# Kernel tuning notes

Hardware: AMD Instinct MI355X
Metric: run time of the kernel (lower is better)

The kernel has to match this reference:

```python
import jax, jax.numpy as jnp
import numpy as np

B, S_ENC, S_DEC = 4, 2048, 1024
ENC_DIM, DEC_DIM, H = 1024, 1024, 16
CROSS_DIM = max(ENC_DIM, DEC_DIM)
HEAD_DIM_DEC = DEC_DIM // H
SCALE = HEAD_DIM_DEC ** 0.5  # module divides by dec_scaling only


def _linear_params(key, d_in, d_out):
    kw, kb = jax.random.split(key)
    bound = 1.0 / np.sqrt(d_in)
    W = jax.random.uniform(kw, (d_in, d_out), jnp.float32, -bound, bound)
    b = jax.random.uniform(kb, (d_out,), jnp.float32, -bound, bound)
    return W, b


def setup_inputs() -> dict:
    key = jax.random.key(0)
    ks = jax.random.split(key, 7)
    enc = jax.random.normal(ks[0], (B, S_ENC, ENC_DIM), jnp.float32)
    dec = jax.random.normal(ks[1], (B, S_DEC, DEC_DIM), jnp.float32)
    enc_mask = jax.random.uniform(ks[2], (B, 1, 1, S_ENC)) < 0.1
    q_w, q_b = _linear_params(ks[3], DEC_DIM, CROSS_DIM)
    k_w, k_b = _linear_params(ks[4], ENC_DIM, CROSS_DIM)
    v_w, v_b = _linear_params(ks[5], ENC_DIM, DEC_DIM)
    o_w, o_b = _linear_params(ks[6], DEC_DIM, DEC_DIM)
    return {"enc": enc, "enc_mask": enc_mask, "dec": dec,
            "q_w": q_w, "q_b": q_b, "k_w": k_w, "k_b": k_b,
            "v_w": v_w, "v_b": v_b, "o_w": o_w, "o_b": o_b}


def _split_heads(x):
    b, s, d = x.shape
    return x.reshape(b, s, H, d // H).transpose(0, 2, 1, 3)  # [b,h,s,hd]


def reference(enc, enc_mask, dec, q_w, q_b, k_w, k_b, v_w, v_b, o_w, o_b):
    q = _split_heads(dec @ q_w + q_b)   # [B,H,Sq,cross_hd]
    k = _split_heads(enc @ k_w + k_b)   # [B,H,Sk,cross_hd]
    v = _split_heads(enc @ v_w + v_b)   # [B,H,Sk,dec_hd]
    logits = jnp.einsum('bhqd,bhkd->bhqk', q, k) / SCALE
    logits = jnp.where(enc_mask, -jnp.inf, logits)
    a = jax.nn.softmax(logits, axis=-1)
    x = jnp.einsum('bhqk,bhkd->bhqd', a, v)          # [B,H,Sq,dec_hd]
    x = x.transpose(0, 2, 1, 3).reshape(x.shape[0], x.shape[2], -1)  # [B,Sq,DEC_DIM]
    return x @ o_w + o_b
```

## Files before the change

### kernel.cpp

```cpp
#include <hip/hip_runtime.h>
#include <hip/hip_bf16.h>
#include <cstdint>

#define BB   4
#define SENC 2048
#define SDEC 1024
#define DM   1024
#define NH   16
#define HD   64

using short8 = __attribute__((ext_vector_type(8))) short;
using f32x4  = __attribute__((ext_vector_type(4))) float;

__device__ inline unsigned short f2bf(float f) {
    return (unsigned short)((__builtin_bit_cast(unsigned int, f) + 0x8000u) >> 16);
}

__device__ inline float fexp2(float x) {
#if __has_builtin(__builtin_amdgcn_exp2f)
    return __builtin_amdgcn_exp2f(x);
#else
    return exp2f(x);
#endif
}

#if __has_builtin(__builtin_amdgcn_global_load_lds)
#define HAS_GLL 1
#endif

__device__ inline void stage16(const void* g, void* l) {
#ifdef HAS_GLL
    typedef __attribute__((address_space(1))) const unsigned int guint;
    typedef __attribute__((address_space(3))) unsigned int luint;
    __builtin_amdgcn_global_load_lds((guint*)g, (luint*)l, 16, 0, 0);
#else
    *(short8*)l = *(const short8*)g;
#endif
}

__global__ __launch_bounds__(256) void cvt_kernel(const float* __restrict__ in,
                                                  unsigned short* __restrict__ out, int n) {
    int i = (blockIdx.x * 256 + threadIdx.x) * 4;
    if (i >= n) return;
    float4 v = *(const float4*)(in + i);
    ushort4 o;
    o.x = f2bf(v.x); o.y = f2bf(v.y); o.z = f2bf(v.z); o.w = f2bf(v.w);
    *(ushort4*)(out + i) = o;
}

__global__ __launch_bounds__(256) void mask_cvt_kernel(const int* __restrict__ m,
                                                       float* __restrict__ mf, int n) {
    int i = blockIdx.x * 256 + threadIdx.x;
    if (i < n) mf[i] = m[i] ? -1e30f : 0.0f;
}

__global__ __launch_bounds__(256) void wtrans_kernel(
    const float* __restrict__ qw, const float* __restrict__ kw,
    const float* __restrict__ vw, const float* __restrict__ ow,
    unsigned short* __restrict__ qwt, unsigned short* __restrict__ kwt,
    unsigned short* __restrict__ vwt, unsigned short* __restrict__ owt) {
    const float* src; unsigned short* dst;
    switch (blockIdx.z) {
        case 0:  src = qw; dst = qwt; break;
        case 1:  src = kw; dst = kwt; break;
        case 2:  src = vw; dst = vwt; break;
        default: src = ow; dst = owt; break;
    }
    __shared__ float t[64][65];
    const int k0 = blockIdx.y * 64, n0 = blockIdx.x * 64;
    const int tid = threadIdx.x;
    #pragma unroll
    for (int it = 0; it < 16; ++it) {
        int e = it * 256 + tid, r = e >> 6, c = e & 63;
        t[r][c] = src[(size_t)(k0 + r) * DM + n0 + c];
    }
    __syncthreads();
    #pragma unroll
    for (int it = 0; it < 16; ++it) {
        int e = it * 256 + tid, r = e >> 6, c = e & 63;
        dst[(size_t)(n0 + r) * DM + k0 + c] = f2bf(t[c][r]);
    }
}

template <int MODE>
__global__ __launch_bounds__(256) void gemm_bt(const unsigned short* __restrict__ A,
                                               const unsigned short* __restrict__ Bt,
                                               const float* __restrict__ bias,
                                               void* __restrict__ Cout) {
    __shared__ unsigned short As[128 * 32];
    __shared__ unsigned short Bs[128 * 32];
    const int tid = threadIdx.x;
    const int wave = tid >> 6, lane = tid & 63, quad = lane >> 4, l16 = lane & 15;
    const int wr = wave >> 1, wc = wave & 1;
    const int m0 = blockIdx.y * 128, n0 = blockIdx.x * 128;
    const int r16 = lane >> 2, c8 = (lane & 3) * 8;
    f32x4 acc[4][4] = {};
    for (int kb = 0; kb < DM; kb += 32) {
        #pragma unroll
        for (int i = 0; i < 2; ++i) {
            const int row = wave * 32 + i * 16 + r16;
            stage16(&A[(size_t)(m0 + row) * DM + kb + c8], &As[row * 32 + c8]);
            stage16(&Bt[(size_t)(n0 + row) * DM + kb + c8], &Bs[row * 32 + c8]);
        }
        __syncthreads();
        short8 af[4], bfr[4];
        #pragma unroll
        for (int i = 0; i < 4; ++i) af[i] = *(const short8*)&As[(wr * 64 + i * 16 + l16) * 32 + quad * 8];
        #pragma unroll
        for (int j = 0; j < 4; ++j) bfr[j] = *(const short8*)&Bs[(wc * 64 + j * 16 + l16) * 32 + quad * 8];
        #pragma unroll
        for (int i = 0; i < 4; ++i)
            #pragma unroll
            for (int j = 0; j < 4; ++j)
                acc[i][j] = __builtin_amdgcn_mfma_f32_16x16x32_bf16(af[i], bfr[j], acc[i][j], 0, 0, 0);
        __syncthreads();
    }
    #pragma unroll
    for (int i = 0; i < 4; ++i) {
        #pragma unroll
        for (int j = 0; j < 4; ++j) {
            const int gc = n0 + wc * 64 + j * 16 + l16;
            const float bv = bias[gc];
            #pragma unroll
            for (int rr = 0; rr < 4; ++rr) {
                const int gr = m0 + wr * 64 + i * 16 + quad * 4 + rr;
                float v = acc[i][j][rr] + bv;
                if (MODE == 0) {
                    int b = gr >> 10, sq = gr & 1023, h = gc >> 6, d = gc & 63;
                    ((unsigned short*)Cout)[(((size_t)(b * NH + h) * SDEC + sq) << 6) + d] = f2bf(v * 0.18033688011112042f);
                } else if (MODE == 1) {
                    int b = gr >> 11, sk = gr & 2047, h = gc >> 6, d = gc & 63;
                    ((unsigned short*)Cout)[(((size_t)(b * NH + h) * SENC + sk) << 6) + d] = f2bf(v);
                } else if (MODE == 2) {
                    int b = gr >> 11, sk = gr & 2047, h = gc >> 6, d = gc & 63;
                    ((unsigned short*)Cout)[((size_t)(b * NH + h) * HD + d) * SENC + sk] = f2bf(v);
                } else {
                    ((float*)Cout)[(size_t)gr * DM + gc] = v;
                }
            }
        }
    }
}

__global__ __launch_bounds__(512) void attn_kernel(const unsigned short* __restrict__ Qb,
                                                   const unsigned short* __restrict__ Kb,
                                                   const unsigned short* __restrict__ Vtb,
                                                   const float* __restrict__ maskf,
                                                   unsigned short* __restrict__ Xb) {
    __shared__ unsigned short Ks[64 * 72];
    __shared__ unsigned short Vs[64 * 72];
    __shared__ unsigned short Ps[8][16 * 72];
    const int bh = blockIdx.y, b = bh >> 4, h = bh & 15;
    const int q0 = blockIdx.x * 128;
    const int tid = threadIdx.x, wave = tid >> 6, lane = tid & 63, quad = lane >> 4, l16 = lane & 15;

    const unsigned short* Qp = Qb + ((size_t)bh * SDEC + q0 + wave * 16) * HD;
    short8 qf0 = *(const short8*)&Qp[l16 * HD + quad * 8];
    short8 qf1 = *(const short8*)&Qp[l16 * HD + 32 + quad * 8];

    const unsigned short* Kp = Kb + (size_t)bh * SENC * HD;
    const unsigned short* Vp = Vtb + (size_t)bh * HD * SENC;
    const float* mp = maskf + (size_t)b * SENC;

    float lsum[4] = {0.f, 0.f, 0.f, 0.f};
    f32x4 o[4] = {};
    const int srow = tid >> 3, scol = (tid & 7) * 8;

    for (int kb = 0; kb < SENC; kb += 64) {
        *(short8*)&Ks[srow * 72 + scol] = *(const short8*)&Kp[(size_t)(kb + srow) * HD + scol];
        *(short8*)&Vs[srow * 72 + scol] = *(const short8*)&Vp[(size_t)srow * SENC + kb + scol];
        __syncthreads();
        f32x4 s[4];
        #pragma unroll
        for (int j = 0; j < 4; ++j) {
            short8 b0 = *(const short8*)&Ks[(j * 16 + l16) * 72 + quad * 8];
            short8 b1 = *(const short8*)&Ks[(j * 16 + l16) * 72 + 32 + quad * 8];
            f32x4 c = {};
            c = __builtin_amdgcn_mfma_f32_16x16x32_bf16(qf0, b0, c, 0, 0, 0);
            c = __builtin_amdgcn_mfma_f32_16x16x32_bf16(qf1, b1, c, 0, 0, 0);
            s[j] = c;
        }
        float mk[4];
        #pragma unroll
        for (int j = 0; j < 4; ++j) mk[j] = mp[kb + j * 16 + l16];
        #pragma unroll
        for (int rr = 0; rr < 4; ++rr) {
            #pragma unroll
            for (int j = 0; j < 4; ++j) {
                float p = fexp2(s[j][rr] + mk[j]);
                lsum[rr] += p;
                Ps[wave][(quad * 4 + rr) * 72 + j * 16 + l16] = f2bf(p);
            }
        }
        asm volatile("s_waitcnt lgkmcnt(0)" ::: "memory");
        short8 pf0 = *(const short8*)&Ps[wave][l16 * 72 + quad * 8];
        short8 pf1 = *(const short8*)&Ps[wave][l16 * 72 + 32 + quad * 8];
        #pragma unroll
        for (int j = 0; j < 4; ++j) {
            short8 v0 = *(const short8*)&Vs[(j * 16 + l16) * 72 + quad * 8];
            short8 v1 = *(const short8*)&Vs[(j * 16 + l16) * 72 + 32 + quad * 8];
            o[j] = __builtin_amdgcn_mfma_f32_16x16x32_bf16(pf0, v0, o[j], 0, 0, 0);
            o[j] = __builtin_amdgcn_mfma_f32_16x16x32_bf16(pf1, v1, o[j], 0, 0, 0);
        }
        __syncthreads();
    }
    float inv[4];
    #pragma unroll
    for (int rr = 0; rr < 4; ++rr) {
        float l = lsum[rr];
        #pragma unroll
        for (int d = 1; d < 16; d <<= 1) l += __shfl_xor(l, d);
        inv[rr] = 1.0f / l;
    }
    #pragma unroll
    for (int j = 0; j < 4; ++j)
        #pragma unroll
        for (int rr = 0; rr < 4; ++rr) {
            int sq = q0 + wave * 16 + quad * 4 + rr;
            Xb[((size_t)(b * SDEC) + sq) * DM + h * HD + j * 16 + l16] = f2bf(o[j][rr] * inv[rr]);
        }
}

extern "C" void kernel_launch(void* const* d_in, const int* in_sizes, int n_in,
                              void* d_out, int out_size, void* d_ws, size_t ws_size,
                              hipStream_t stream) {
    const float* enc   = (const float*)d_in[0];
    const int*   emask = (const int*)d_in[1];
    const float* dec   = (const float*)d_in[2];
    const float* q_w   = (const float*)d_in[3];
    const float* q_b   = (const float*)d_in[4];
    const float* k_w   = (const float*)d_in[5];
    const float* k_b   = (const float*)d_in[6];
    const float* v_w   = (const float*)d_in[7];
    const float* v_b   = (const float*)d_in[8];
    const float* o_w   = (const float*)d_in[9];
    const float* o_b   = (const float*)d_in[10];
    float* out = (float*)d_out;

    char* ws = (char*)d_ws;
    unsigned short* decb = (unsigned short*)ws; ws += (size_t)4096 * 1024 * 2;
    unsigned short* encb = (unsigned short*)ws; ws += (size_t)8192 * 1024 * 2;
    unsigned short* qwt  = (unsigned short*)ws; ws += (size_t)1024 * 1024 * 2;
    unsigned short* kwt  = (unsigned short*)ws; ws += (size_t)1024 * 1024 * 2;
    unsigned short* vwt  = (unsigned short*)ws; ws += (size_t)1024 * 1024 * 2;
    unsigned short* owt  = (unsigned short*)ws; ws += (size_t)1024 * 1024 * 2;
    unsigned short* Qb   = (unsigned short*)ws; ws += (size_t)BB * NH * SDEC * HD * 2;
    unsigned short* Kb   = (unsigned short*)ws; ws += (size_t)BB * NH * SENC * HD * 2;
    unsigned short* Vtb  = (unsigned short*)ws; ws += (size_t)BB * NH * HD * SENC * 2;
    unsigned short* Xb   = (unsigned short*)ws; ws += (size_t)4096 * 1024 * 2;
    float*          mkf  = (float*)ws;          ws += (size_t)BB * SENC * 4;

    cvt_kernel<<<4096, 256, 0, stream>>>(dec, decb, 4096 * 1024);
    cvt_kernel<<<8192, 256, 0, stream>>>(enc, encb, 8192 * 1024);
    mask_cvt_kernel<<<32, 256, 0, stream>>>(emask, mkf, BB * SENC);
    wtrans_kernel<<<dim3(16, 16, 4), 256, 0, stream>>>(q_w, k_w, v_w, o_w, qwt, kwt, vwt, owt);
    gemm_bt<0><<<dim3(8, 32), 256, 0, stream>>>(decb, qwt, q_b, (void*)Qb);
    gemm_bt<1><<<dim3(8, 64), 256, 0, stream>>>(encb, kwt, k_b, (void*)Kb);
    gemm_bt<2><<<dim3(8, 64), 256, 0, stream>>>(encb, vwt, v_b, (void*)Vtb);
    attn_kernel<<<dim3(8, 64), 512, 0, stream>>>(Qb, Kb, Vtb, mkf, Xb);
    gemm_bt<3><<<dim3(8, 32), 256, 0, stream>>>(Xb, owt, o_b, (void*)out);
}
```

Before: 300.2 us.

## Merge QKV GEMMs and conversions, double-buffer attention with two query groups per wave

Merges the dec and enc conversions into one launch and folds the mask conversion into the attention kernel, which now reads the int mask directly. The Q, K and V projections become a single launch of 1280 blocks over a concatenated K/V weight. Attention now runs 256 threads, each wave handling 32 query rows against K/V tiles that are double-buffered in LDS via global_load_lds. P is written with packed bf16 stores, and softmax row sums are reduced with fewer shuffles. The aim is to cut launch count and per-tile load latency, at the cost of more registers per wave and a different LDS layout that may conflict.

Result: no change. 299.8 us (-0.1%).

```diff
diff --git a/kernel.cpp b/kernel.cpp
--- a/kernel.cpp
+++ b/kernel.cpp
@@ -14,6 +14,10 @@
 
 __device__ inline unsigned short f2bf(float f) {
     return (unsigned short)((__builtin_bit_cast(unsigned int, f) + 0x8000u) >> 16);
+}
+__device__ inline unsigned int pk2bf(float a, float b) {
+    return ((__builtin_bit_cast(unsigned int, a) + 0x8000u) >> 16) |
+           ((__builtin_bit_cast(unsigned int, b) + 0x8000u) & 0xffff0000u);
 }
 
 __device__ inline float fexp2(float x) {
@@ -38,32 +42,28 @@
 #endif
 }
 
-__global__ __launch_bounds__(256) void cvt_kernel(const float* __restrict__ in,
-                                                  unsigned short* __restrict__ out, int n) {
+__global__ __launch_bounds__(256) void cvt2_kernel(const float* __restrict__ dec,
+                                                   const float* __restrict__ enc,
+                                                   unsigned short* __restrict__ out) {
+    const int nd = BB * SDEC * DM;
     int i = (blockIdx.x * 256 + threadIdx.x) * 4;
-    if (i >= n) return;
-    float4 v = *(const float4*)(in + i);
+    const float* src = (i < nd) ? (dec + i) : (enc + (i - nd));
+    float4 v = *(const float4*)src;
     ushort4 o;
     o.x = f2bf(v.x); o.y = f2bf(v.y); o.z = f2bf(v.z); o.w = f2bf(v.w);
     *(ushort4*)(out + i) = o;
 }
 
-__global__ __launch_bounds__(256) void mask_cvt_kernel(const int* __restrict__ m,
-                                                       float* __restrict__ mf, int n) {
-    int i = blockIdx.x * 256 + threadIdx.x;
-    if (i < n) mf[i] = m[i] ? -1e30f : 0.0f;
-}
-
 __global__ __launch_bounds__(256) void wtrans_kernel(
     const float* __restrict__ qw, const float* __restrict__ kw,
     const float* __restrict__ vw, const float* __restrict__ ow,
-    unsigned short* __restrict__ qwt, unsigned short* __restrict__ kwt,
-    unsigned short* __restrict__ vwt, unsigned short* __restrict__ owt) {
+    unsigned short* __restrict__ qwt, unsigned short* __restrict__ kvwt,
+    unsigned short* __restrict__ owt) {
     const float* src; unsigned short* dst;
     switch (blockIdx.z) {
         case 0:  src = qw; dst = qwt; break;
-        case 1:  src = kw; dst = kwt; break;
-        case 2:  src = vw; dst = vwt; break;
+        case 1:  src = kw; dst = kvwt; break;
+        case 2:  src = vw; dst = kvwt + (size_t)1024 * DM; break;
         default: src = ow; dst = owt; break;
     }
     __shared__ float t[64][65];
@@ -82,13 +82,76 @@
     }
 }
 
-template <int MODE>
-__global__ __launch_bounds__(256) void gemm_bt(const unsigned short* __restrict__ A,
-                                               const unsigned short* __restrict__ Bt,
-                                               const float* __restrict__ bias,
-                                               void* __restrict__ Cout) {
-    __shared__ unsigned short As[128 * 32];
-    __shared__ unsigned short Bs[128 * 32];
+__global__ __launch_bounds__(256) void gemm_qkv_kernel(
+    const unsigned short* __restrict__ encb, const unsigned short* __restrict__ decb,
+    const unsigned short* __restrict__ kvwt, const unsigned short* __restrict__ qwt,
+    const float* __restrict__ q_b, const float* __restrict__ k_b, const float* __restrict__ v_b,
+    unsigned short* __restrict__ Qb, unsigned short* __restrict__ Kb,
+    unsigned short* __restrict__ Vtb) {
+    __shared__ __align__(16) unsigned short As[128 * 32];
+    __shared__ __align__(16) unsigned short Bs[128 * 32];
+    const int id = blockIdx.x;
+    const bool isKV = id < 1024;
+    const unsigned short *A, *Bt;
+    int m0, n0;
+    if (isKV) { A = encb; Bt = kvwt; m0 = (id >> 4) * 128; n0 = (id & 15) * 128; }
+    else      { int i2 = id - 1024; A = decb; Bt = qwt; m0 = (i2 >> 3) * 128; n0 = (i2 & 7) * 128; }
+    const int tid = threadIdx.x;
+    const int wave = tid >> 6, lane = tid & 63, quad = lane >> 4, l16 = lane & 15;
+    const int wr = wave >> 1, wc = wave & 1;
+    const int r16 = lane >> 2, c8 = (lane & 3) * 8;
+    f32x4 acc[4][4] = {};
+    for (int kb = 0; kb < DM; kb += 32) {
+        #pragma unroll
+        for (int i = 0; i < 2; ++i) {
+            const int row = wave * 32 + i * 16 + r16;
+            stage16(&A[(size_t)(m0 + row) * DM + kb + c8], &As[row * 32 + c8]);
+            stage16(&Bt[(size_t)(n0 + row) * DM + kb + c8], &Bs[row * 32 + c8]);
+        }
+        __syncthreads();
+        short8 af[4], bfr[4];
+        #pragma unroll
+        for (int i = 0; i < 4; ++i) af[i] = *(const short8*)&As[(wr * 64 + i * 16 + l16) * 32 + quad * 8];
+        #pragma unroll
+        for (int j = 0; j < 4; ++j) bfr[j] = *(const short8*)&Bs[(wc * 64 + j * 16 + l16) * 32 + quad * 8];
+        #pragma unroll
+        for (int i = 0; i < 4; ++i)
+            #pragma unroll
+            for (int j = 0; j < 4; ++j)
+                acc[i][j] = __builtin_amdgcn_mfma_f32_16x16x32_bf16(af[i], bfr[j], acc[i][j], 0, 0, 0);
+        __syncthreads();
+    }
+    #pragma unroll
+    for (int i = 0; i < 4; ++i) {
+        #pragma unroll
+        for (int j = 0; j < 4; ++j) {
+            const int gc = n0 + wc * 64 + j * 16 + l16;
+            #pragma unroll
+            for (int rr = 0; rr < 4; ++rr) {
+                const int gr = m0 + wr * 64 + i * 16 + quad * 4 + rr;
+                if (!isKV) {
+                    int b = gr >> 10, sq = gr & 1023, h = gc >> 6, d = gc & 63;
+                    float v = (acc[i][j][rr] + q_b[gc]) * 0.18033688011112042f;
+                    Qb[(((size_t)(b * NH + h) * SDEC + sq) << 6) + d] = f2bf(v);
+                } else if (gc < 1024) {
+                    int b = gr >> 11, sk = gr & 2047, h = gc >> 6, d = gc & 63;
+                    Kb[(((size_t)(b * NH + h) * SENC + sk) << 6) + d] = f2bf(acc[i][j][rr] + k_b[gc]);
+                } else {
+                    int gc2 = gc & 1023;
+                    int b = gr >> 11, sk = gr & 2047, h = gc2 >> 6, d = gc2 & 63;
+                    Vtb[((size_t)(b * NH + h) * HD + d) * SENC + sk] = f2bf(acc[i][j][rr] + v_b[gc2]);
+                }
+            }
+        }
+    }
+}
+
+__global__ __launch_bounds__(256) void gemm_o_kernel(const unsigned short* __restrict__ A,
+                                                     const unsigned short* __restrict__ Bt,
+                                                     const float* __restrict__ bias,
+                                                     float* __restrict__ Cout) {
+    __shared__ __align__(16) unsigned short As[128 * 32];
+    __shared__ __align__(16) unsigned short Bs[128 * 32];
     const int tid = threadIdx.x;
     const int wave = tid >> 6, lane = tid & 63, quad = lane >> 4, l16 = lane & 15;
     const int wr = wave >> 1, wc = wave & 1;
@@ -116,7 +179,7 @@
         __syncthreads();
     }
     #pragma unroll
-    for (int i = 0; i < 4; ++i) {
+    for (int i = 0; i < 4; ++i)
         #pragma unroll
         for (int j = 0; j < 4; ++j) {
             const int gc = n0 + wc * 64 + j * 16 + l16;
@@ -124,101 +187,120 @@
             #pragma unroll
             for (int rr = 0; rr < 4; ++rr) {
                 const int gr = m0 + wr * 64 + i * 16 + quad * 4 + rr;
-                float v = acc[i][j][rr] + bv;
-                if (MODE == 0) {
-                    int b = gr >> 10, sq = gr & 1023, h = gc >> 6, d = gc & 63;
-                    ((unsigned short*)Cout)[(((size_t)(b * NH + h) * SDEC + sq) << 6) + d] = f2bf(v * 0.18033688011112042f);
-                } else if (MODE == 1) {
-                    int b = gr >> 11, sk = gr & 2047, h = gc >> 6, d = gc & 63;
-                    ((unsigned short*)Cout)[(((size_t)(b * NH + h) * SENC + sk) << 6) + d] = f2bf(v);
-                } else if (MODE == 2) {
-                    int b = gr >> 11, sk = gr & 2047, h = gc >> 6, d = gc & 63;
-                    ((unsigned short*)Cout)[((size_t)(b * NH + h) * HD + d) * SENC + sk] = f2bf(v);
-                } else {
-                    ((float*)Cout)[(size_t)gr * DM + gc] = v;
-                }
-            }
-        }
-    }
-}
-
-__global__ __launch_bounds__(512) void attn_kernel(const unsigned short* __restrict__ Qb,
-                                                   const unsigned short* __restrict__ Kb,
-                                                   const unsigned short* __restrict__ Vtb,
-                                                   const float* __restrict__ maskf,
-                                                   unsigned short* __restrict__ Xb) {
-    __shared__ unsigned short Ks[64 * 72];
-    __shared__ unsigned short Vs[64 * 72];
-    __shared__ unsigned short Ps[8][16 * 72];
+                Cout[(size_t)gr * DM + gc] = acc[i][j][rr] + bv;
+            }
+        }
+}
+
+__global__ __launch_bounds__(256, 2) void attn_kernel(const unsigned short* __restrict__ Qb,
+                                                      const unsigned short* __restrict__ Kb,
+                                                      const unsigned short* __restrict__ Vtb,
+                                                      const int* __restrict__ mask,
+                                                      unsigned short* __restrict__ Xb) {
+    __shared__ __align__(16) unsigned short Ks[2][2][64 * 32];
+    __shared__ __align__(16) unsigned short Vs[2][2][64 * 32];
+    __shared__ __align__(16) unsigned short Ps[4][16 * 72];
     const int bh = blockIdx.y, b = bh >> 4, h = bh & 15;
     const int q0 = blockIdx.x * 128;
-    const int tid = threadIdx.x, wave = tid >> 6, lane = tid & 63, quad = lane >> 4, l16 = lane & 15;
-
-    const unsigned short* Qp = Qb + ((size_t)bh * SDEC + q0 + wave * 16) * HD;
-    short8 qf0 = *(const short8*)&Qp[l16 * HD + quad * 8];
-    short8 qf1 = *(const short8*)&Qp[l16 * HD + 32 + quad * 8];
+    const int tid = threadIdx.x, wave = tid >> 6, lane = tid & 63;
+    const int quad = lane >> 4, l16 = lane & 15;
+    const int sr = lane >> 2, sc = (lane & 3) * 8;
 
     const unsigned short* Kp = Kb + (size_t)bh * SENC * HD;
     const unsigned short* Vp = Vtb + (size_t)bh * HD * SENC;
-    const float* mp = maskf + (size_t)b * SENC;
-
-    float lsum[4] = {0.f, 0.f, 0.f, 0.f};
-    f32x4 o[4] = {};
-    const int srow = tid >> 3, scol = (tid & 7) * 8;
-
-    for (int kb = 0; kb < SENC; kb += 64) {
-        *(short8*)&Ks[srow * 72 + scol] = *(const short8*)&Kp[(size_t)(kb + srow) * HD + scol];
-        *(short8*)&Vs[srow * 72 + scol] = *(const short8*)&Vp[(size_t)srow * SENC + kb + scol];
-        __syncthreads();
-        f32x4 s[4];
+    const int* mp = mask + (size_t)b * SENC;
+
+    short8 qf[2][2];
+    {
+        const unsigned short* Qp = Qb + ((size_t)bh * SDEC + q0 + wave * 32) * HD;
+        #pragma unroll
+        for (int g = 0; g < 2; ++g) {
+            qf[g][0] = *(const short8*)&Qp[(g * 16 + l16) * HD + quad * 8];
+            qf[g][1] = *(const short8*)&Qp[(g * 16 + l16) * HD + 32 + quad * 8];
+        }
+    }
+
+    float lsum[2] = {0.f, 0.f};
+    f32x4 o[2][4] = {};
+
+    {
+        const unsigned short* kg = Kp + (size_t)(wave * 16 + sr) * HD;
+        stage16(kg + sc,      &Ks[0][0][(wave * 16 + sr) * 32 + sc]);
+        stage16(kg + 32 + sc, &Ks[0][1][(wave * 16 + sr) * 32 + sc]);
+        const unsigned short* vg = Vp + (size_t)(wave * 16 + sr) * SENC;
+        stage16(vg + sc,      &Vs[0][0][(wave * 16 + sr) * 32 + sc]);
+        stage16(vg + 32 + sc, &Vs[0][1][(wave * 16 + sr) * 32 + sc]);
+    }
+
+    for (int it = 0; it < SENC / 64; ++it) {
+        const int bf = it & 1;
+        __syncthreads();
+        if (it + 1 < SENC / 64) {
+            const int nb = bf ^ 1, kb2 = (it + 1) * 64;
+            const unsigned short* kg = Kp + (size_t)(kb2 + wave * 16 + sr) * HD;
+            stage16(kg + sc,      &Ks[nb][0][(wave * 16 + sr) * 32 + sc]);
+            stage16(kg + 32 + sc, &Ks[nb][1][(wave * 16 + sr) * 32 + sc]);
+            const unsigned short* vg = Vp + (size_t)(wave * 16 + sr) * SENC + kb2;
+            stage16(vg + sc,      &Vs[nb][0][(wave * 16 + sr) * 32 + sc]);
+            stage16(vg + 32 + sc, &Vs[nb][1][(wave * 16 + sr) * 32 + sc]);
+        }
+        const int kb = it * 64;
+        short8 kA0[4], kA1[4], vB0[4], vB1[4];
         #pragma unroll
         for (int j = 0; j < 4; ++j) {
-            short8 b0 = *(const short8*)&Ks[(j * 16 + l16) * 72 + quad * 8];
-            short8 b1 = *(const short8*)&Ks[(j * 16 + l16) * 72 + 32 + quad * 8];
-            f32x4 c = {};
-            c = __builtin_amdgcn_mfma_f32_16x16x32_bf16(qf0, b0, c, 0, 0, 0);
-            c = __builtin_amdgcn_mfma_f32_16x16x32_bf16(qf1, b1, c, 0, 0, 0);
-            s[j] = c;
-        }
-        float mk[4];
-        #pragma unroll
-        for (int j = 0; j < 4; ++j) mk[j] = mp[kb + j * 16 + l16];
+            kA0[j] = *(const short8*)&Ks[bf][0][(j * 16 + l16) * 32 + quad * 8];
+            kA1[j] = *(const short8*)&Ks[bf][1][(j * 16 + l16) * 32 + quad * 8];
+            vB0[j] = *(const short8*)&Vs[bf][0][(j * 16 + l16) * 32 + quad * 8];
+            vB1[j] = *(const short8*)&Vs[bf][1][(j * 16 + l16) * 32 + quad * 8];
+        }
+        int4 mi[4];
+        #pragma unroll
+        for (int j = 0; j < 4; ++j) mi[j] = *(const int4*)&mp[kb + j * 16 + quad * 4];
+        #pragma unroll
+        for (int g = 0; g < 2; ++g) {
+            f32x4 st[4];
+            #pragma unroll
+            for (int j = 0; j < 4; ++j) {
+                f32x4 z = {0.f, 0.f, 0.f, 0.f};
+                z = __builtin_amdgcn_mfma_f32_16x16x32_bf16(kA0[j], qf[g][0], z, 0, 0, 0);
+                st[j] = __builtin_amdgcn_mfma_f32_16x16x32_bf16(kA1[j], qf[g][1], z, 0, 0, 0);
+            }
+            #pragma unroll
+            for (int j = 0; j < 4; ++j) {
+                float p0 = mi[j].x ? 0.f : fexp2(st[j][0]);
+                float p1 = mi[j].y ? 0.f : fexp2(st[j][1]);
+                float p2 = mi[j].z ? 0.f : fexp2(st[j][2]);
+                float p3 = mi[j].w ? 0.f : fexp2(st[j][3]);
+                lsum[g] += (p0 + p1) + (p2 + p3);
+                uint2 pkv;
+                pkv.x = pk2bf(p0, p1);
+                pkv.y = pk2bf(p2, p3);
+                *(uint2*)&Ps[wave][l16 * 72 + j * 16 + quad * 4] = pkv;
+            }
+            asm volatile("s_waitcnt lgkmcnt(0)" ::: "memory");
+            short8 pA0 = *(const short8*)&Ps[wave][l16 * 72 + quad * 8];
+            short8 pA1 = *(const short8*)&Ps[wave][l16 * 72 + 32 + quad * 8];
+            #pragma unroll
+            for (int dj = 0; dj < 4; ++dj) {
+                o[g][dj] = __builtin_amdgcn_mfma_f32_16x16x32_bf16(pA0, vB0[dj], o[g][dj], 0, 0, 0);
+                o[g][dj] = __builtin_amdgcn_mfma_f32_16x16x32_bf16(pA1, vB1[dj], o[g][dj], 0, 0, 0);
+            }
+        }
+    }
+    #pragma unroll
+    for (int g = 0; g < 2; ++g) {
+        float lg = lsum[g];
+        lg += __shfl_xor(lg, 16);
+        lg += __shfl_xor(lg, 32);
         #pragma unroll
         for (int rr = 0; rr < 4; ++rr) {
-            #pragma unroll
-            for (int j = 0; j < 4; ++j) {
-                float p = fexp2(s[j][rr] + mk[j]);
-                lsum[rr] += p;
-                Ps[wave][(quad * 4 + rr) * 72 + j * 16 + l16] = f2bf(p);
-            }
-        }
-        asm volatile("s_waitcnt lgkmcnt(0)" ::: "memory");
-        short8 pf0 = *(const short8*)&Ps[wave][l16 * 72 + quad * 8];
-        short8 pf1 = *(const short8*)&Ps[wave][l16 * 72 + 32 + quad * 8];
-        #pragma unroll
-        for (int j = 0; j < 4; ++j) {
-            short8 v0 = *(const short8*)&Vs[(j * 16 + l16) * 72 + quad * 8];
-            short8 v1 = *(const short8*)&Vs[(j * 16 + l16) * 72 + 32 + quad * 8];
-            o[j] = __builtin_amdgcn_mfma_f32_16x16x32_bf16(pf0, v0, o[j], 0, 0, 0);
-            o[j] = __builtin_amdgcn_mfma_f32_16x16x32_bf16(pf1, v1, o[j], 0, 0, 0);
-        }
-        __syncthreads();
-    }
-    float inv[4];
-    #pragma unroll
-    for (int rr = 0; rr < 4; ++rr) {
-        float l = lsum[rr];
-        #pragma unroll
-        for (int d = 1; d < 16; d <<= 1) l += __shfl_xor(l, d);
-        inv[rr] = 1.0f / l;
-    }
-    #pragma unroll
-    for (int j = 0; j < 4; ++j)
-        #pragma unroll
-        for (int rr = 0; rr < 4; ++rr) {
-            int sq = q0 + wave * 16 + quad * 4 + rr;
-            Xb[((size_t)(b * SDEC) + sq) * DM + h * HD + j * 16 + l16] = f2bf(o[j][rr] * inv[rr]);
-        }
+            float iv = 1.0f / __shfl(lg, quad * 4 + rr, 64);
+            int sq = q0 + wave * 32 + g * 16 + quad * 4 + rr;
+            #pragma unroll
+            for (int dj = 0; dj < 4; ++dj)
+                Xb[((size_t)(b * SDEC) + sq) * DM + h * HD + dj * 16 + l16] = f2bf(o[g][dj][rr] * iv);
+        }
+    }
 }
 
 extern "C" void kernel_launch(void* const* d_in, const int* in_sizes, int n_in,
@@ -241,22 +323,16 @@
     unsigned short* decb = (unsigned short*)ws; ws += (size_t)4096 * 1024 * 2;
     unsigned short* encb = (unsigned short*)ws; ws += (size_t)8192 * 1024 * 2;
     unsigned short* qwt  = (unsigned short*)ws; ws += (size_t)1024 * 1024 * 2;
-    unsigned short* kwt  = (unsigned short*)ws; ws += (size_t)1024 * 1024 * 2;
-    unsigned short* vwt  = (unsigned short*)ws; ws += (size_t)1024 * 1024 * 2;
+    unsigned short* kvwt = (unsigned short*)ws; ws += (size_t)2048 * 1024 * 2;
     unsigned short* owt  = (unsigned short*)ws; ws += (size_t)1024 * 1024 * 2;
     unsigned short* Qb   = (unsigned short*)ws; ws += (size_t)BB * NH * SDEC * HD * 2;
     unsigned short* Kb   = (unsigned short*)ws; ws += (size_t)BB * NH * SENC * HD * 2;
     unsigned short* Vtb  = (unsigned short*)ws; ws += (size_t)BB * NH * HD * SENC * 2;
     unsigned short* Xb   = (unsigned short*)ws; ws += (size_t)4096 * 1024 * 2;
-    float*          mkf  = (float*)ws;          ws += (size_t)BB * SENC * 4;
-
-    cvt_kernel<<<4096, 256, 0, stream>>>(dec, decb, 4096 * 1024);
-    cvt_kernel<<<8192, 256, 0, stream>>>(enc, encb, 8192 * 1024);
-    mask_cvt_kernel<<<32, 256, 0, stream>>>(emask, mkf, BB * SENC);
-    wtrans_kernel<<<dim3(16, 16, 4), 256, 0, stream>>>(q_w, k_w, v_w, o_w, qwt, kwt, vwt, owt);
-    gemm_bt<0><<<dim3(8, 32), 256, 0, stream>>>(decb, qwt, q_b, (void*)Qb);
-    gemm_bt<1><<<dim3(8, 64), 256, 0, stream>>>(encb, kwt, k_b, (void*)Kb);
-    gemm_bt<2><<<dim3(8, 64), 256, 0, stream>>>(encb, vwt, v_b, (void*)Vtb);
-    attn_kernel<<<dim3(8, 64), 512, 0, stream>>>(Qb, Kb, Vtb, mkf, Xb);
-    gemm_bt<3><<<dim3(8, 32), 256, 0, stream>>>(Xb, owt, o_b, (void*)out);
-}
+
+    cvt2_kernel<<<12288, 256, 0, stream>>>(dec, enc, decb);
+    wtrans_kernel<<<dim3(16, 16, 4), 256, 0, stream>>>(q_w, k_w, v_w, o_w, qwt, kvwt, owt);
+    gemm_qkv_kernel<<<1280, 256, 0, stream>>>(encb, decb, kvwt, qwt, q_b, k_b, v_b, Qb, Kb, Vtb);
+    attn_kernel<<<dim3(8, 64), 256, 0, stream>>>(Qb, Kb, Vtb, emask, Xb);
+    gemm_o_kernel<<<dim3(8, 32), 256, 0, stream>>>(Xb, owt, o_b, out);
+}
```
